# Kernel tuning notes

Hardware: AMD Instinct MI355X
Metric: run time of the kernel (lower is better)

Reference implementation:

```python
import jax, jax.numpy as jnp
import numpy as np

N = 50000          # nodes
E = 1_600_000      # edges (avg degree 32)
F_IN = 256
F_OUT = 256
ALPHA = 0.2        # LeakyReLU negative slope


def setup_inputs() -> dict:
    key = jax.random.key(0)
    ks = jax.random.split(key, 7)
    x = jax.random.normal(ks[0], (N, F_IN), dtype=jnp.float32)
    row = jax.random.randint(ks[1], (E,), 0, N, dtype=jnp.int32)  # dst i
    col = jax.random.randint(ks[2], (E,), 0, N, dtype=jnp.int32)  # src j
    W_w = jax.random.normal(ks[3], (F_IN, F_OUT), dtype=jnp.float32) / np.sqrt(F_IN).astype(np.float32)
    W_b = jax.random.normal(ks[4], (F_OUT,), dtype=jnp.float32) * 0.01
    a_w = jax.random.normal(ks[5], (2 * F_OUT,), dtype=jnp.float32) / np.sqrt(2 * F_OUT).astype(np.float32)
    a_b = jax.random.normal(ks[6], (1,), dtype=jnp.float32) * 0.01
    return {"x": x, "W_w": W_w, "W_b": W_b, "a_w": a_w, "a_b": a_b,
            "row": row, "col": col}


def reference(x, W_w, W_b, a_w, a_b, row, col):
    # Wh = W(x): [N, F_OUT]
    Wh = x @ W_w + W_b
    # e[i,j] = leakyrelu(a1 . Wh[j] + a2 . Wh[i] + b)
    # (repeat puts Wh[j] in the first half of the concat, repeat_interleave Wh[i] in the second)
    f_dst_part = Wh @ a_w[:F_OUT]   # contribution of column node j
    f_row_part = Wh @ a_w[F_OUT:]   # contribution of row node i
    e = f_dst_part[col] + f_row_part[row] + a_b[0]          # [E]
    e = jnp.where(e > 0, e, ALPHA * e)                      # LeakyReLU
    # sparse softmax over dim=1 (segment = row i), adjacency values are 1.0
    m = jax.ops.segment_max(e, row, num_segments=N)         # [N]
    ex = jnp.exp(e - m[row])
    denom = jax.ops.segment_sum(ex, row, num_segments=N)    # [N]
    att = ex / denom[row]                                   # [E]
    # h'[i] = sum_j att[i,j] * Wh[j]  (spmm), empty rows stay zero
    h_prime = jax.ops.segment_sum(att[:, None] * Wh[col], row, num_segments=N)
    return jax.nn.relu(h_prime)
```

## Files before the change

kernel.cpp:

```cpp
#include <hip/hip_runtime.h>
#include <math.h>

#define N_NODES 50000
#define N_EDGES 1600000
#define F 256
#define ALPHA 0.2f
#define NP 50048
#define NB 196
#define CAP 10240
#define EPB 4096
#define NAB ((N_EDGES + EPB - 1) / EPB)
#define UNROLL 16
#define GEMM_BLOCKS 782
#define FVEC_BLOCKS ((N_NODES + 3) / 4)

typedef short bf16x8 __attribute__((ext_vector_type(8)));
typedef float f32x4 __attribute__((ext_vector_type(4)));
typedef _Float16 half4 __attribute__((ext_vector_type(4)));

__device__ __forceinline__ unsigned short f2bf(float f) {
  union { float f; unsigned u; } v; v.f = f;
  unsigned u = v.u;
  return (unsigned short)((u + 0x7fffu + ((u >> 16) & 1u)) >> 16);
}

__device__ __forceinline__ unsigned short f2h_bits(float f) {
  union { _Float16 h; unsigned short u; } v;
  v.h = (_Float16)f;
  return v.u;
}

__device__ __forceinline__ float h_bits2f(unsigned short u) {
  union { _Float16 h; unsigned short u; } v;
  v.u = u;
  return (float)v.h;
}

__global__ __launch_bounds__(256) void prep_w(const float* __restrict__ W,
                                              const float* __restrict__ a_w,
                                              const float* __restrict__ W_b,
                                              const float* __restrict__ a_b,
                                              unsigned short* __restrict__ Wt,
                                              float* __restrict__ wa,
                                              float* __restrict__ cb) {
  const int lane = threadIdx.x & 63, w = threadIdx.x >> 6;
  const int k = blockIdx.x * 4 + w;
  float4 wv = *(const float4*)(W + (size_t)k * F + lane * 4);
  float4 a1 = *(const float4*)(a_w + lane * 4);
  float4 a2 = *(const float4*)(a_w + F + lane * 4);
  Wt[(size_t)(lane * 4 + 0) * F + k] = f2bf(wv.x);
  Wt[(size_t)(lane * 4 + 1) * F + k] = f2bf(wv.y);
  Wt[(size_t)(lane * 4 + 2) * F + k] = f2bf(wv.z);
  Wt[(size_t)(lane * 4 + 3) * F + k] = f2bf(wv.w);
  float s1 = wv.x * a1.x + wv.y * a1.y + wv.z * a1.z + wv.w * a1.w;
  float s2 = wv.x * a2.x + wv.y * a2.y + wv.z * a2.z + wv.w * a2.w;
#pragma unroll
  for (int off = 32; off > 0; off >>= 1) {
    s1 += __shfl_down(s1, off, 64);
    s2 += __shfl_down(s2, off, 64);
  }
  if (lane == 0) { wa[k] = s1; wa[F + k] = s2; }
  if (blockIdx.x == 0 && w == 0) {
    float4 b = *(const float4*)(W_b + lane * 4);
    float t1 = b.x * (a1.x + a2.x) + b.y * (a1.y + a2.y) +
               b.z * (a1.z + a2.z) + b.w * (a1.w + a2.w);
#pragma unroll
    for (int off = 32; off > 0; off >>= 1) t1 += __shfl_down(t1, off, 64);
    if (lane == 0) cb[0] = t1 + a_b[0];
  }
}

__global__ __launch_bounds__(256) void fvec2_binA2(
    const float* __restrict__ x,
    const float* __restrict__ wa,
    const int* __restrict__ row,
    const int* __restrict__ col,
    float* __restrict__ f_dst,
    float* __restrict__ f_row,
    unsigned short* __restrict__ x_bf,
    int* __restrict__ gcur,
    unsigned* __restrict__ gstage) {
  if (blockIdx.x < NAB) {
    __shared__ int h[NB], lofs[NB], lcur[NB], gb[NB];
    __shared__ unsigned stage[EPB];
    const int t = threadIdx.x;
    for (int i = t; i < NB; i += 256) { h[i] = 0; lcur[i] = 0; }
    __syncthreads();
    const int base = blockIdx.x * EPB;
    const int cnt = min(EPB, N_EDGES - base);
#pragma unroll
    for (int j = 0; j < 16; ++j) {
      int k = base + j * 256 + t;
      if (k < N_EDGES) atomicAdd(&h[row[k] >> 8], 1);
    }
    __syncthreads();
    if (t == 0) {
      int run = 0;
      for (int i = 0; i < NB; ++i) { lofs[i] = run; run += h[i]; }
    }
    __syncthreads();
    if (t < NB && h[t] > 0) gb[t] = atomicAdd(&gcur[t], h[t]);
    __syncthreads();
#pragma unroll
    for (int j = 0; j < 16; ++j) {
      int k = base + j * 256 + t;
      if (k < N_EDGES) {
        int r = row[k], b = r >> 8;
        int lp = lofs[b] + atomicAdd(&lcur[b], 1);
        stage[lp] = ((unsigned)b << 24) | ((unsigned)(r & 255) << 16) |
                    (unsigned)col[k];
      }
    }
    __syncthreads();
#pragma unroll
    for (int j = 0; j < 16; ++j) {
      int s = j * 256 + t;
      if (s < cnt) {
        unsigned wv = stage[s];
        int b = wv >> 24;
        gstage[(size_t)b * CAP + gb[b] + (s - lofs[b])] = wv & 0x00FFFFFFu;
      }
    }
    return;
  }
  const int lane = threadIdx.x & 63, w = threadIdx.x >> 6;
  const int node = (blockIdx.x - NAB) * 4 + w;
  if (node >= N_NODES) return;
  float4 xv = *(const float4*)(x + (size_t)node * F + lane * 4);
  ushort4 xb;
  xb.x = f2bf(xv.x); xb.y = f2bf(xv.y); xb.z = f2bf(xv.z); xb.w = f2bf(xv.w);
  *(ushort4*)(x_bf + (size_t)node * F + lane * 4) = xb;
  float4 v1 = *(const float4*)(wa + lane * 4);
  float4 v2 = *(const float4*)(wa + F + lane * 4);
  float s1 = xv.x * v1.x + xv.y * v1.y + xv.z * v1.z + xv.w * v1.w;
  float s2 = xv.x * v2.x + xv.y * v2.y + xv.z * v2.z + xv.w * v2.w;
#pragma unroll
  for (int off = 32; off > 0; off >>= 1) {
    s1 += __shfl_down(s1, off, 64);
    s2 += __shfl_down(s2, off, 64);
  }
  if (lane == 0) { f_dst[node] = s1; f_row[node] = s2; }
}

#define LDSK 72
__global__ __launch_bounds__(256) void gemm_binB(
    const unsigned short* __restrict__ Xb,
    const unsigned short* __restrict__ Wt,
    const float* __restrict__ bias,
    _Float16* __restrict__ Wh,
    const int* __restrict__ gcur,
    const unsigned* __restrict__ gstage,
    const float* __restrict__ f_dst,
    const float* __restrict__ f_row,
    const float* __restrict__ cb,
    int2* __restrict__ rsc,
    float* __restrict__ inv_denom,
    unsigned* __restrict__ csr) {
  __shared__ char smem[2 * 128 * LDSK * 2];
  if (blockIdx.x < NB) {
    int* cnt = (int*)smem;
    int* cur = cnt + 256;
    float* dsum = (float*)(cur + 256);
    const int t = threadIdx.x;
    const int b = blockIdx.x;
    cnt[t] = 0;
    dsum[t] = 0.f;
    __syncthreads();
    const int nb = gcur[b];
    const int start = b * CAP;
    const float cbs = cb[0];
    for (int s = t; s < nb; s += 256) {
      unsigned wv = gstage[start + s];
      atomicAdd(&cnt[(wv >> 16) & 255], 1);
    }
    __syncthreads();
    if (t == 0) {
      int run = 0;
      for (int i = 0; i < 256; ++i) { int v = cnt[i]; cur[i] = run; run += v; }
    }
    __syncthreads();
    const int gr = (b << 8) + t;
    if (gr < N_NODES) rsc[gr] = make_int2(start + cur[t], cnt[t]);
    __syncthreads();
    for (int s = t; s < nb; s += 256) {
      unsigned wv = gstage[start + s];
      int lr = (wv >> 16) & 255;
      int c = wv & 0xFFFF;
      float ev = f_dst[c] + f_row[(b << 8) + lr] + cbs;
      ev = ev > 0.f ? ev : ALPHA * ev;
      float ex = __expf(ev);
      int p = start + atomicAdd(&cur[lr], 1);
      csr[p] = ((unsigned)f2h_bits(ex) << 16) | (unsigned)c;
      atomicAdd(&dsum[lr], ex);
    }
    __syncthreads();
    if (gr < N_NODES)
      inv_denom[gr] = (cnt[t] > 0) ? (1.0f / dsum[t]) : 0.f;
    return;
  }
  short* As = (short*)smem;
  short* Bs = As + 128 * LDSK;
  const int bid = blockIdx.x - NB;
  const int tid = threadIdx.x;
  const int lane = tid & 63;
  const int w = tid >> 6;
  const int wm = w >> 1, wn = w & 1;
  const int m0 = (bid >> 1) * 128;
  const int n0 = (bid & 1) * 128;
  f32x4 acc[4][4] = {{{0.f, 0.f, 0.f, 0.f}}};
  const int srow = tid >> 3;
  const int schunk = tid & 7;

  for (int k0 = 0; k0 < F; k0 += 64) {
#pragma unroll
    for (int i = 0; i < 4; ++i) {
      int r = i * 32 + srow;
      int gm = m0 + r; if (gm > N_NODES - 1) gm = N_NODES - 1;
      *(bf16x8*)&As[r * LDSK + schunk * 8] =
          *(const bf16x8*)(Xb + (size_t)gm * F + k0 + schunk * 8);
      *(bf16x8*)&Bs[r * LDSK + schunk * 8] =
          *(const bf16x8*)(Wt + (size_t)(n0 + r) * F + k0 + schunk * 8);
    }
    __syncthreads();
#pragma unroll
    for (int kk = 0; kk < 64; kk += 32) {
      const int rowsel = lane & 15;
      const int ksel = kk + (lane >> 4) * 8;
      bf16x8 af[4], bfr[4];
#pragma unroll
      for (int t = 0; t < 4; ++t) {
        af[t] = *(bf16x8*)&As[(wm * 64 + t * 16 + rowsel) * LDSK + ksel];
        bfr[t] = *(bf16x8*)&Bs[(wn * 64 + t * 16 + rowsel) * LDSK + ksel];
      }
#pragma unroll
      for (int mi = 0; mi < 4; ++mi)
#pragma unroll
        for (int nj = 0; nj < 4; ++nj)
          acc[mi][nj] = __builtin_amdgcn_mfma_f32_16x16x32_bf16(
              af[mi], bfr[nj], acc[mi][nj], 0, 0, 0);
    }
    __syncthreads();
  }
  const int crow = (lane >> 4) * 4;
  const int ccol = lane & 15;
#pragma unroll
  for (int nj = 0; nj < 4; ++nj) {
    int gc = n0 + wn * 64 + nj * 16 + ccol;
    float bv = bias[gc];
#pragma unroll
    for (int mi = 0; mi < 4; ++mi) {
      int gr = m0 + wm * 64 + mi * 16 + crow;
#pragma unroll
      for (int r = 0; r < 4; ++r)
        Wh[(size_t)(gr + r) * F + gc] = (_Float16)(acc[mi][nj][r] + bv);
    }
  }
}

__global__ __launch_bounds__(256) void gat_pull(const int2* __restrict__ rsc,
                                                const unsigned* __restrict__ csr,
                                                const float* __restrict__ inv_denom,
                                                const _Float16* __restrict__ Wh,
                                                float* __restrict__ out) {
  const int lane = threadIdx.x & 63, w = threadIdx.x >> 6;
  const int i = blockIdx.x * 4 + w;
  if (i >= N_NODES) return;
  const int2 rc = rsc[i];
  const int s = rc.x, e = rc.x + rc.y;
  const char* whb = (const char*)Wh;
  const unsigned laneoff = (unsigned)lane * 8u;
  float4 acc = make_float4(0.f, 0.f, 0.f, 0.f);
  for (int p = s; p < e; p += UNROLL) {
    unsigned wv[UNROLL];
#pragma unroll
    for (int j = 0; j < UNROLL; ++j) {
      int q = p + j;
      wv[j] = csr[q < e ? q : s];
    }
    half4 v[UNROLL];
#pragma unroll
    for (int j = 0; j < UNROLL; ++j) {
      unsigned off = (wv[j] & 0xFFFFu) * 512u + laneoff;
      v[j] = *(const half4*)(whb + off);
    }
#pragma unroll
    for (int j = 0; j < UNROLL; ++j) {
      float xw = h_bits2f((unsigned short)(wv[j] >> 16));
      xw = (p + j < e) ? xw : 0.f;
      acc.x += xw * (float)v[j][0];
      acc.y += xw * (float)v[j][1];
      acc.z += xw * (float)v[j][2];
      acc.w += xw * (float)v[j][3];
    }
  }
  const float inv = inv_denom[i];
  acc.x = fmaxf(acc.x * inv, 0.f); acc.y = fmaxf(acc.y * inv, 0.f);
  acc.z = fmaxf(acc.z * inv, 0.f); acc.w = fmaxf(acc.w * inv, 0.f);
  ((float4*)out)[(size_t)i * 64 + lane] = acc;
}

extern "C" void kernel_launch(void* const* d_in, const int* in_sizes, int n_in,
                              void* d_out, int out_size, void* d_ws, size_t ws_size,
                              hipStream_t stream) {
  const float* x   = (const float*)d_in[0];
  const float* W_w = (const float*)d_in[1];
  const float* W_b = (const float*)d_in[2];
  const float* a_w = (const float*)d_in[3];
  const float* a_b = (const float*)d_in[4];
  const int*   row = (const int*)d_in[5];
  const int*   col = (const int*)d_in[6];
  float* out = (float*)d_out;

  float* ws = (float*)d_ws;
  size_t off = 0;
  _Float16* Wh = (_Float16*)(ws + off); off += (size_t)NP * F / 2;
  unsigned short* x_bf = (unsigned short*)(ws + off); off += (size_t)NP * F / 2;
  unsigned short* Wt = (unsigned short*)(ws + off); off += (F * F) / 2;
  float* wa = ws + off;            off += 2 * F;
  float* cb = ws + off;            off += 8;
  float* f_dst = ws + off;         off += NP;
  float* f_row = ws + off;         off += NP;
  int* gcur = (int*)(ws + off);    off += NB;
  int2* rsc = (int2*)(ws + off);   off += 2 * (size_t)NP;
  float* inv_denom = (float*)(ws + off); off += NP;
  unsigned* gstage = (unsigned*)(ws + off); off += (size_t)NB * CAP;
  unsigned* csr = (unsigned*)(ws + off); off += (size_t)NB * CAP;
  (void)ws_size; (void)in_sizes; (void)n_in; (void)out_size;

  hipMemsetAsync(gcur, 0, NB * sizeof(int), stream);

  hipLaunchKernelGGL(prep_w, dim3(64), dim3(256), 0, stream, W_w, a_w, W_b,
                     a_b, Wt, wa, cb);
  hipLaunchKernelGGL(fvec2_binA2, dim3(NAB + FVEC_BLOCKS), dim3(256), 0,
                     stream, x, wa, row, col, f_dst, f_row, x_bf, gcur, gstage);
  hipLaunchKernelGGL(gemm_binB, dim3(NB + GEMM_BLOCKS), dim3(256), 0, stream,
                     x_bf, Wt, W_b, Wh, gcur, gstage, f_dst, f_row, cb, rsc,
                     inv_denom, csr);
  hipLaunchKernelGGL(gat_pull, dim3((N_NODES + 3) / 4), dim3(256), 0, stream,
                     rsc, csr, inv_denom, Wh, out);
}
```

Measured before the change: 282.0 us.

## Fuse fp32-to-bf16 conversion into GEMM and regroup kernel stages

The GEMM now reads fp32 x directly and converts it to bf16 while staging tiles into shared memory, so the separate x_bf buffer and its write/read round trip are gone. The GEMM moves into the same launch as the edge binning and f-vector blocks. The second binning pass becomes its own 512-thread kernel, and the gcur memset is folded into an extra prep_w block. This removes about 50 MB of intermediate traffic and a memset call, at the cost of more global load bytes per GEMM tile and redundant x reads across the two N-tiles.

```diff
diff --git a/kernel.cpp b/kernel.cpp
--- a/kernel.cpp
+++ b/kernel.cpp
@@ -42,7 +42,12 @@
                                               const float* __restrict__ a_b,
                                               unsigned short* __restrict__ Wt,
                                               float* __restrict__ wa,
-                                              float* __restrict__ cb) {
+                                              float* __restrict__ cb,
+                                              int* __restrict__ gcur) {
+  if (blockIdx.x == 64) {
+    if (threadIdx.x < NB) gcur[threadIdx.x] = 0;
+    return;
+  }
   const int lane = threadIdx.x & 63, w = threadIdx.x >> 6;
   const int k = blockIdx.x * 4 + w;
   float4 wv = *(const float4*)(W + (size_t)k * F + lane * 4);
@@ -70,23 +75,95 @@
   }
 }
 
-__global__ __launch_bounds__(256) void fvec2_binA2(
+#define LDSK 72
+__global__ __launch_bounds__(256) void gemm_fvec_binA2(
     const float* __restrict__ x,
+    const unsigned short* __restrict__ Wt,
+    const float* __restrict__ bias,
     const float* __restrict__ wa,
     const int* __restrict__ row,
     const int* __restrict__ col,
+    _Float16* __restrict__ Wh,
     float* __restrict__ f_dst,
     float* __restrict__ f_row,
-    unsigned short* __restrict__ x_bf,
     int* __restrict__ gcur,
     unsigned* __restrict__ gstage) {
-  if (blockIdx.x < NAB) {
-    __shared__ int h[NB], lofs[NB], lcur[NB], gb[NB];
-    __shared__ unsigned stage[EPB];
+  __shared__ char smem[2 * 128 * LDSK * 2];
+  if (blockIdx.x < GEMM_BLOCKS) {
+    short* As = (short*)smem;
+    short* Bs = As + 128 * LDSK;
+    const int tid = threadIdx.x;
+    const int lane = tid & 63;
+    const int w = tid >> 6;
+    const int wm = w >> 1, wn = w & 1;
+    const int m0 = (blockIdx.x >> 1) * 128;
+    const int n0 = (blockIdx.x & 1) * 128;
+    f32x4 acc[4][4] = {{{0.f, 0.f, 0.f, 0.f}}};
+    const int srow = tid >> 3;
+    const int schunk = tid & 7;
+    for (int k0 = 0; k0 < F; k0 += 64) {
+#pragma unroll
+      for (int i = 0; i < 4; ++i) {
+        int r = i * 32 + srow;
+        int gm = m0 + r; if (gm > N_NODES - 1) gm = N_NODES - 1;
+        const float* src = x + (size_t)gm * F + k0 + schunk * 8;
+        float4 lo = *(const float4*)src;
+        float4 hi = *(const float4*)(src + 4);
+        bf16x8 v;
+        v[0] = (short)f2bf(lo.x); v[1] = (short)f2bf(lo.y);
+        v[2] = (short)f2bf(lo.z); v[3] = (short)f2bf(lo.w);
+        v[4] = (short)f2bf(hi.x); v[5] = (short)f2bf(hi.y);
+        v[6] = (short)f2bf(hi.z); v[7] = (short)f2bf(hi.w);
+        *(bf16x8*)&As[r * LDSK + schunk * 8] = v;
+        *(bf16x8*)&Bs[r * LDSK + schunk * 8] =
+            *(const bf16x8*)(Wt + (size_t)(n0 + r) * F + k0 + schunk * 8);
+      }
+      __syncthreads();
+#pragma unroll
+      for (int kk = 0; kk < 64; kk += 32) {
+        const int rowsel = lane & 15;
+        const int ksel = kk + (lane >> 4) * 8;
+        bf16x8 af[4], bfr[4];
+#pragma unroll
+        for (int t = 0; t < 4; ++t) {
+          af[t] = *(bf16x8*)&As[(wm * 64 + t * 16 + rowsel) * LDSK + ksel];
+          bfr[t] = *(bf16x8*)&Bs[(wn * 64 + t * 16 + rowsel) * LDSK + ksel];
+        }
+#pragma unroll
+        for (int mi = 0; mi < 4; ++mi)
+#pragma unroll
+          for (int nj = 0; nj < 4; ++nj)
+            acc[mi][nj] = __builtin_amdgcn_mfma_f32_16x16x32_bf16(
+                af[mi], bfr[nj], acc[mi][nj], 0, 0, 0);
+      }
+      __syncthreads();
+    }
+    const int crow = (lane >> 4) * 4;
+    const int ccol = lane & 15;
+#pragma unroll
+    for (int nj = 0; nj < 4; ++nj) {
+      int gc = n0 + wn * 64 + nj * 16 + ccol;
+      float bv = bias[gc];
+#pragma unroll
+      for (int mi = 0; mi < 4; ++mi) {
+        int gr = m0 + wm * 64 + mi * 16 + crow;
+#pragma unroll
+        for (int r = 0; r < 4; ++r)
+          Wh[(size_t)(gr + r) * F + gc] = (_Float16)(acc[mi][nj][r] + bv);
+      }
+    }
+    return;
+  }
+  if (blockIdx.x < GEMM_BLOCKS + NAB) {
+    int* h = (int*)smem;
+    int* lofs = h + NB;
+    int* lcur = lofs + NB;
+    int* gb = lcur + NB;
+    unsigned* stage = (unsigned*)(gb + NB);
     const int t = threadIdx.x;
     for (int i = t; i < NB; i += 256) { h[i] = 0; lcur[i] = 0; }
     __syncthreads();
-    const int base = blockIdx.x * EPB;
+    const int base = (blockIdx.x - GEMM_BLOCKS) * EPB;
     const int cnt = min(EPB, N_EDGES - base);
 #pragma unroll
     for (int j = 0; j < 16; ++j) {
@@ -124,12 +201,9 @@
     return;
   }
   const int lane = threadIdx.x & 63, w = threadIdx.x >> 6;
-  const int node = (blockIdx.x - NAB) * 4 + w;
+  const int node = (blockIdx.x - GEMM_BLOCKS - NAB) * 4 + w;
   if (node >= N_NODES) return;
   float4 xv = *(const float4*)(x + (size_t)node * F + lane * 4);
-  ushort4 xb;
-  xb.x = f2bf(xv.x); xb.y = f2bf(xv.y); xb.z = f2bf(xv.z); xb.w = f2bf(xv.w);
-  *(ushort4*)(x_bf + (size_t)node * F + lane * 4) = xb;
   float4 v1 = *(const float4*)(wa + lane * 4);
   float4 v2 = *(const float4*)(wa + F + lane * 4);
   float s1 = xv.x * v1.x + xv.y * v1.y + xv.z * v1.z + xv.w * v1.w;
@@ -142,118 +216,53 @@
   if (lane == 0) { f_dst[node] = s1; f_row[node] = s2; }
 }
 
-#define LDSK 72
-__global__ __launch_bounds__(256) void gemm_binB(
-    const unsigned short* __restrict__ Xb,
-    const unsigned short* __restrict__ Wt,
-    const float* __restrict__ bias,
-    _Float16* __restrict__ Wh,
-    const int* __restrict__ gcur,
-    const unsigned* __restrict__ gstage,
-    const float* __restrict__ f_dst,
-    const float* __restrict__ f_row,
-    const float* __restrict__ cb,
-    int2* __restrict__ rsc,
-    float* __restrict__ inv_denom,
-    unsigned* __restrict__ csr) {
-  __shared__ char smem[2 * 128 * LDSK * 2];
-  if (blockIdx.x < NB) {
-    int* cnt = (int*)smem;
-    int* cur = cnt + 256;
-    float* dsum = (float*)(cur + 256);
-    const int t = threadIdx.x;
-    const int b = blockIdx.x;
-    cnt[t] = 0;
-    dsum[t] = 0.f;
-    __syncthreads();
-    const int nb = gcur[b];
-    const int start = b * CAP;
-    const float cbs = cb[0];
-    for (int s = t; s < nb; s += 256) {
-      unsigned wv = gstage[start + s];
-      atomicAdd(&cnt[(wv >> 16) & 255], 1);
-    }
-    __syncthreads();
-    if (t == 0) {
-      int run = 0;
-      for (int i = 0; i < 256; ++i) { int v = cnt[i]; cur[i] = run; run += v; }
-    }
-    __syncthreads();
-    const int gr = (b << 8) + t;
-    if (gr < N_NODES) rsc[gr] = make_int2(start + cur[t], cnt[t]);
-    __syncthreads();
-    for (int s = t; s < nb; s += 256) {
-      unsigned wv = gstage[start + s];
-      int lr = (wv >> 16) & 255;
-      int c = wv & 0xFFFF;
-      float ev = f_dst[c] + f_row[(b << 8) + lr] + cbs;
-      ev = ev > 0.f ? ev : ALPHA * ev;
-      float ex = __expf(ev);
-      int p = start + atomicAdd(&cur[lr], 1);
-      csr[p] = ((unsigned)f2h_bits(ex) << 16) | (unsigned)c;
-      atomicAdd(&dsum[lr], ex);
-    }
-    __syncthreads();
-    if (gr < N_NODES)
-      inv_denom[gr] = (cnt[t] > 0) ? (1.0f / dsum[t]) : 0.f;
-    return;
-  }
-  short* As = (short*)smem;
-  short* Bs = As + 128 * LDSK;
-  const int bid = blockIdx.x - NB;
-  const int tid = threadIdx.x;
-  const int lane = tid & 63;
-  const int w = tid >> 6;
-  const int wm = w >> 1, wn = w & 1;
-  const int m0 = (bid >> 1) * 128;
-  const int n0 = (bid & 1) * 128;
-  f32x4 acc[4][4] = {{{0.f, 0.f, 0.f, 0.f}}};
-  const int srow = tid >> 3;
-  const int schunk = tid & 7;
-
-  for (int k0 = 0; k0 < F; k0 += 64) {
-#pragma unroll
-    for (int i = 0; i < 4; ++i) {
-      int r = i * 32 + srow;
-      int gm = m0 + r; if (gm > N_NODES - 1) gm = N_NODES - 1;
-      *(bf16x8*)&As[r * LDSK + schunk * 8] =
-          *(const bf16x8*)(Xb + (size_t)gm * F + k0 + schunk * 8);
-      *(bf16x8*)&Bs[r * LDSK + schunk * 8] =
-          *(const bf16x8*)(Wt + (size_t)(n0 + r) * F + k0 + schunk * 8);
-    }
-    __syncthreads();
-#pragma unroll
-    for (int kk = 0; kk < 64; kk += 32) {
-      const int rowsel = lane & 15;
-      const int ksel = kk + (lane >> 4) * 8;
-      bf16x8 af[4], bfr[4];
-#pragma unroll
-      for (int t = 0; t < 4; ++t) {
-        af[t] = *(bf16x8*)&As[(wm * 64 + t * 16 + rowsel) * LDSK + ksel];
-        bfr[t] = *(bf16x8*)&Bs[(wn * 64 + t * 16 + rowsel) * LDSK + ksel];
-      }
-#pragma unroll
-      for (int mi = 0; mi < 4; ++mi)
-#pragma unroll
-        for (int nj = 0; nj < 4; ++nj)
-          acc[mi][nj] = __builtin_amdgcn_mfma_f32_16x16x32_bf16(
-              af[mi], bfr[nj], acc[mi][nj], 0, 0, 0);
-    }
-    __syncthreads();
-  }
-  const int crow = (lane >> 4) * 4;
-  const int ccol = lane & 15;
-#pragma unroll
-  for (int nj = 0; nj < 4; ++nj) {
-    int gc = n0 + wn * 64 + nj * 16 + ccol;
-    float bv = bias[gc];
-#pragma unroll
-    for (int mi = 0; mi < 4; ++mi) {
-      int gr = m0 + wm * 64 + mi * 16 + crow;
-#pragma unroll
-      for (int r = 0; r < 4; ++r)
-        Wh[(size_t)(gr + r) * F + gc] = (_Float16)(acc[mi][nj][r] + bv);
-    }
+__global__ __launch_bounds__(512) void binB(const int* __restrict__ gcur,
+                                            const unsigned* __restrict__ gstage,
+                                            const float* __restrict__ f_dst,
+                                            const float* __restrict__ f_row,
+                                            const float* __restrict__ cb,
+                                            int2* __restrict__ rsc,
+                                            float* __restrict__ inv_denom,
+                                            unsigned* __restrict__ csr) {
+  __shared__ int cnt[256], cur[256];
+  __shared__ float dsum[256];
+  const int t = threadIdx.x;
+  const int b = blockIdx.x;
+  if (t < 256) { cnt[t] = 0; dsum[t] = 0.f; }
+  __syncthreads();
+  const int nb = gcur[b];
+  const int start = b * CAP;
+  const float cbs = cb[0];
+  for (int s = t; s < nb; s += 512) {
+    unsigned wv = gstage[start + s];
+    atomicAdd(&cnt[(wv >> 16) & 255], 1);
+  }
+  __syncthreads();
+  if (t == 0) {
+    int run = 0;
+    for (int i = 0; i < 256; ++i) { int v = cnt[i]; cur[i] = run; run += v; }
+  }
+  __syncthreads();
+  if (t < 256) {
+    int g = (b << 8) + t;
+    if (g < N_NODES) rsc[g] = make_int2(start + cur[t], cnt[t]);
+  }
+  __syncthreads();
+  for (int s = t; s < nb; s += 512) {
+    unsigned wv = gstage[start + s];
+    int lr = (wv >> 16) & 255;
+    int c = wv & 0xFFFF;
+    float ev = f_dst[c] + f_row[(b << 8) + lr] + cbs;
+    ev = ev > 0.f ? ev : ALPHA * ev;
+    float ex = __expf(ev);
+    int p = start + atomicAdd(&cur[lr], 1);
+    csr[p] = ((unsigned)f2h_bits(ex) << 16) | (unsigned)c;
+    atomicAdd(&dsum[lr], ex);
+  }
+  __syncthreads();
+  if (t < 256) {
+    int g = (b << 8) + t;
+    if (g < N_NODES) inv_denom[g] = (cnt[t] > 0) ? (1.0f / dsum[t]) : 0.f;
   }
 }
 
@@ -314,7 +323,6 @@
   float* ws = (float*)d_ws;
   size_t off = 0;
   _Float16* Wh = (_Float16*)(ws + off); off += (size_t)NP * F / 2;
-  unsigned short* x_bf = (unsigned short*)(ws + off); off += (size_t)NP * F / 2;
   unsigned short* Wt = (unsigned short*)(ws + off); off += (F * F) / 2;
   float* wa = ws + off;            off += 2 * F;
   float* cb = ws + off;            off += 8;
@@ -327,15 +335,13 @@
   unsigned* csr = (unsigned*)(ws + off); off += (size_t)NB * CAP;
   (void)ws_size; (void)in_sizes; (void)n_in; (void)out_size;
 
-  hipMemsetAsync(gcur, 0, NB * sizeof(int), stream);
-
-  hipLaunchKernelGGL(prep_w, dim3(64), dim3(256), 0, stream, W_w, a_w, W_b,
-                     a_b, Wt, wa, cb);
-  hipLaunchKernelGGL(fvec2_binA2, dim3(NAB + FVEC_BLOCKS), dim3(256), 0,
-                     stream, x, wa, row, col, f_dst, f_row, x_bf, gcur, gstage);
-  hipLaunchKernelGGL(gemm_binB, dim3(NB + GEMM_BLOCKS), dim3(256), 0, stream,
-                     x_bf, Wt, W_b, Wh, gcur, gstage, f_dst, f_row, cb, rsc,
-                     inv_denom, csr);
+  hipLaunchKernelGGL(prep_w, dim3(65), dim3(256), 0, stream, W_w, a_w, W_b,
+                     a_b, Wt, wa, cb, gcur);
+  hipLaunchKernelGGL(gemm_fvec_binA2, dim3(GEMM_BLOCKS + NAB + FVEC_BLOCKS),
+                     dim3(256), 0, stream, x, Wt, W_b, wa, row, col, Wh,
+                     f_dst, f_row, gcur, gstage);
+  hipLaunchKernelGGL(binB, dim3(NB), dim3(512), 0, stream, gcur, gstage,
+                     f_dst, f_row, cb, rsc, inv_denom, csr);
   hipLaunchKernelGGL(gat_pull, dim3((N_NODES + 3) / 4), dim3(256), 0, stream,
                      rsc, csr, inv_denom, Wh, out);
 }
```

Measured after the change: 289.2 us. 1.03x slower.
